# Performance work log

Measured on AMD Instinct MI355X. Metric: run time of the kernel, lower is better.

## Reference

```python
import jax, jax.numpy as jnp
import numpy as np

# Dimensions (see shape_source): B batches, W walks, L walk length, N anonymized node-id space
B, W, L, N = 256, 128, 20, 64
SIGMA = 2.0  # CooccurrenceMatrix(sigma=2.0)


def setup_inputs() -> dict:
    key = jax.random.key(0)
    k1, k2 = jax.random.split(key)
    anonymized_nodes = jax.random.randint(k1, (B, W, L), 0, N, dtype=jnp.int32)
    walk_masks = jax.random.randint(k2, (B, W, L), 0, 2).astype(bool)
    # Gaussian positional kernel buffer: kernel[i,j] = exp(-(i-j)^2 / sigma^2)
    pos = jnp.arange(L, dtype=jnp.float32)
    kernel = jnp.exp(-((pos[:, None] - pos[None, :]) ** 2) / (SIGMA ** 2))
    return {"anonymized_nodes": anonymized_nodes, "walk_masks": walk_masks, "kernel": kernel}


def reference(anonymized_nodes, walk_masks, kernel):
    # Faithful vectorized form of CooccurrenceMatrix.forward.
    # Original: per batch, group valid (walk,pos) entries by node id (sort +
    # change-points); for each group with >=2 entries, scatter-add
    # kernel[pos_i, pos_j] into cooccurrence[b, walk_i, walk_j] for all pairs
    # (i,j) in the group (including i==j). Then normalize by outer product of
    # walk lengths, clamp, tanh.
    valid = walk_masks.astype(jnp.float32)                     # [B,W,L]
    # T[b,w,l,n] = 1 if entry (w,l) is valid and holds node id n
    T = jax.nn.one_hot(anonymized_nodes, N, dtype=jnp.float32) * valid[..., None]  # [B,W,L,N]
    # Segments with < 2 occurrences contribute nothing (original skips them)
    cnt = T.sum(axis=(1, 2))                                   # [B,N]
    T = T * (cnt >= 2.0).astype(jnp.float32)[:, None, None, :]
    K = jnp.clip(kernel, -10.0, 10.0)                          # clamp as in _add_segment_deterministic
    # cooccurrence[b,w,v] = sum_n sum_{l,m} T[b,w,l,n] K[l,m] T[b,v,m,n]
    S = jnp.einsum('bwln,lm->bwmn', T, K)                      # [B,W,L,N]
    cooc = jnp.einsum('bwmn,bvmn->bwv', S, T)                  # [B,W,W]
    # Normalization by walk-length outer product
    walk_lens = valid.sum(-1)                                  # [B,W]
    norm = jnp.clip(walk_lens[:, :, None] * walk_lens[:, None, :], 1e-6, None)
    valid_pairs = (walk_lens[:, :, None] > 0) & (walk_lens[:, None, :] > 0)
    cooc = jnp.where(valid_pairs, cooc / norm, 0.0)
    return jnp.tanh(jnp.clip(cooc, -10.0, 10.0))
```

## Files before the change

kernel.cpp:

```cpp
#include <hip/hip_runtime.h>
#include <hip/hip_bf16.h>

#define BB   256
#define W    128
#define L    20
#define NN   64
#define WL   (W * L)
#define NT   1024
#define CS   129
#define NSLOT 3
#define NKEY (L * NN)
#define DLMAX 4

__global__ __launch_bounds__(NT) void cooc_kernel(
    const int* __restrict__ nodes,
    const void* __restrict__ masks,
    const float* __restrict__ kern,
    float* __restrict__ out)
{
    __shared__ __align__(16) float cooc[W * CS];
    __shared__ unsigned ent[WL];
    __shared__ unsigned hist[NKEY];
    __shared__ unsigned offs[NKEY];
    __shared__ unsigned long long maskS[40];
    __shared__ unsigned long long maskD[40];
    __shared__ int cnt[NN];
    __shared__ __align__(16) int wlen[W];
    __shared__ float diagC[W];
    __shared__ int totS;

    const int tid = threadIdx.x;
    const int b = blockIdx.x;
    const int base = b * WL;

    const unsigned mword = ((const unsigned*)masks)[tid];
    int nval[NSLOT];
    #pragma unroll
    for (int k = 0; k < NSLOT; k++) {
        int e = tid + k * NT;
        nval[k] = (e < WL) ? nodes[base + e] : 0;
    }

    hist[tid] = 0;
    if (tid + NT < NKEY) hist[tid + NT] = 0;
    {
        float4* c4 = (float4*)cooc;
        for (int i = tid; i < (W * CS) / 4; i += NT)
            c4[i] = make_float4(0.f, 0.f, 0.f, 0.f);
    }
    int flag;
    {
        unsigned v = mword;
        unsigned long long b0 = __ballot(v > 1u);
        unsigned long long b1 = __ballot(v != 0u && v != 0x3F800000u);
        unsigned long long b2 = __ballot(v != 0u && v != 0x3F80u && v != 0x3F800000u &&
                                         v != 0x3F803F80u && v != 0x3C00u &&
                                         v != 0x3C000000u && v != 0x3C003C00u);
        flag = b0 ? (b1 ? (b2 ? 1 : 3) : 2) : 0;
        flag = __builtin_amdgcn_readfirstlane(flag);
    }
    __syncthreads();

    bool vld[NSLOT];
    {
        const int e0 = tid, e1 = tid + NT, e2 = tid + 2 * NT;
        const bool g2 = (e2 < WL);
        if (flag == 0) {
            const int* m = (const int*)masks;
            vld[0] = m[base + e0] != 0;
            vld[1] = m[base + e1] != 0;
            vld[2] = g2 ? (m[base + e2] != 0) : false;
        } else if (flag == 2) {
            const float* m = (const float*)masks;
            vld[0] = m[base + e0] != 0.f;
            vld[1] = m[base + e1] != 0.f;
            vld[2] = g2 ? (m[base + e2] != 0.f) : false;
        } else if (flag == 3) {
            const unsigned short* m = (const unsigned short*)masks;
            vld[0] = m[base + e0] != 0;
            vld[1] = m[base + e1] != 0;
            vld[2] = g2 ? (m[base + e2] != 0) : false;
        } else {
            const unsigned char* m = (const unsigned char*)masks;
            vld[0] = m[base + e0] != 0;
            vld[1] = m[base + e1] != 0;
            vld[2] = g2 ? (m[base + e2] != 0) : false;
        }
    }

    unsigned eval[NSLOT];
    int      kreg[NSLOT];
    unsigned plocal[NSLOT];
    #pragma unroll
    for (int k = 0; k < NSLOT; k++) {
        int e = tid + k * NT;
        bool valid = vld[k];
        eval[k] = 0xFFFFFFFFu;
        kreg[k] = 0;
        plocal[k] = 0;
        if (valid) {
            int n = nval[k] & (NN - 1);
            int w = e / L;
            int l = e - w * L;
            eval[k] = ((unsigned)n << 12) | ((unsigned)l << 7) | (unsigned)w;
            kreg[k] = l * NN + n;
        }
        unsigned long long bal = __ballot(valid);
        int widx = k * 16 + (tid >> 6);
        if ((tid & 63) == 0 && widx < 40) maskS[widx] = bal;
        if (valid) plocal[k] = atomicAdd(&hist[kreg[k]], 1u);
    }
    __syncthreads();

    if (tid < NN) {
        int tl[L];
        int s = 0;
        #pragma unroll
        for (int l = 0; l < L; l++) { tl[l] = (int)hist[l * NN + tid]; s += tl[l]; }
        cnt[tid] = s;
        int inc = s;
        #pragma unroll
        for (int d = 1; d < NN; d <<= 1) {
            int t = __shfl_up(inc, d, 64);
            if (tid >= d) inc += t;
        }
        int run = inc - s;
        if (tid == NN - 1) totS = inc;
        #pragma unroll
        for (int l = 0; l < L; l++) {
            int idx = l * NN + tid;
            offs[idx] = (unsigned)run;
            run += tl[l];
            hist[idx] = (unsigned)run;
        }
    }
    if (tid < W) {
        int bit0 = tid * L;
        int i0 = bit0 >> 6, sh = bit0 & 63;
        unsigned long long m = maskS[i0] >> sh;
        if (sh > 64 - L) m |= maskS[i0 + 1] << (64 - sh);
        wlen[tid] = __popcll(m & 0xFFFFFu);
    }
    __syncthreads();

    #pragma unroll
    for (int k = 0; k < NSLOT; k++) {
        bool d2 = false;
        if (eval[k] != 0xFFFFFFFFu) {
            ent[offs[kreg[k]] + plocal[k]] = eval[k];
            d2 = (cnt[(int)(eval[k] >> 12)] >= 2);
        }
        unsigned long long bal = __ballot(d2);
        int widx = k * 16 + (tid >> 6);
        if ((tid & 63) == 0 && widx < 40) maskD[widx] = bal;
    }
    __syncthreads();

    if (tid < W) {
        int bit0 = tid * L;
        int i0 = bit0 >> 6, sh = bit0 & 63;
        unsigned long long m = maskD[i0] >> sh;
        if (sh > 64 - L) m |= maskD[i0 + 1] << (64 - sh);
        diagC[tid] = (float)__popcll(m & 0xFFFFFu);
    }

    const float KC = -0.360673760222f;
    const int tot = totS;
    #pragma unroll
    for (int k = 0; k < NSLOT; k++) {
        const int p = tid + k * NT;
        if (p >= tot) continue;
        const unsigned e = ent[p];
        const int n = (int)(e >> 12);
        const int l1 = (int)((e >> 7) & 31u);
        const int w1row = (int)(e & 127u) * CS;
        const int lmax = (l1 + DLMAX < L - 1) ? (l1 + DLMAX) : (L - 1);
        const int jend = (int)hist[lmax * NN + n];
        const int jm = jend - 1;
        for (int j = p + 1; j < jend; j += 4) {
            int j1 = (j + 1 < jm) ? j + 1 : jm;
            int j2 = (j + 2 < jm) ? j + 2 : jm;
            int j3 = (j + 3 < jm) ? j + 3 : jm;
            unsigned ea = ent[j];
            unsigned eb = ent[j1];
            unsigned ec = ent[j2];
            unsigned ed = ent[j3];
            int da = (int)((ea >> 7) & 31u) - l1;
            int db = (int)((eb >> 7) & 31u) - l1;
            int dc = (int)((ec >> 7) & 31u) - l1;
            int dd = (int)((ed >> 7) & 31u) - l1;
            float ka = __builtin_amdgcn_exp2f((float)(da * da) * KC);
            float kb = __builtin_amdgcn_exp2f((float)(db * db) * KC);
            float kc = __builtin_amdgcn_exp2f((float)(dc * dc) * KC);
            float kd = __builtin_amdgcn_exp2f((float)(dd * dd) * KC);
            atomicAdd(&cooc[w1row + (int)(ea & 127u)], ka);
            if (j + 1 <= jm) atomicAdd(&cooc[w1row + (int)(eb & 127u)], kb);
            if (j + 2 <= jm) atomicAdd(&cooc[w1row + (int)(ec & 127u)], kc);
            if (j + 3 <= jm) atomicAdd(&cooc[w1row + (int)(ed & 127u)], kd);
        }
    }
    __syncthreads();

    for (int s4 = 0; s4 < (W * W) / (NT * 4); s4++) {
        const int i = (tid + s4 * NT) * 4;
        const int wr = i >> 7;
        const int v = i & (W - 1);
        const float4 row = *(const float4*)&cooc[wr * CS + v];
        const int4 lv4 = *(const int4*)&wlen[v];
        const int lw = wlen[wr];
        float rr[4] = {row.x, row.y, row.z, row.w};
        float tt[4] = {cooc[(v + 0) * CS + wr], cooc[(v + 1) * CS + wr],
                       cooc[(v + 2) * CS + wr], cooc[(v + 3) * CS + wr]};
        int lv[4] = {lv4.x, lv4.y, lv4.z, lv4.w};
        float o[4];
        #pragma unroll
        for (int u = 0; u < 4; u++) {
            float s = rr[u] + tt[u];
            if (v + u == wr) s += diagC[wr];
            float nrm = (float)(lw * lv[u]);
            float x = s * __builtin_amdgcn_rcpf(fmaxf(nrm, 1e-6f));
            x = fminf(fmaxf(x, -10.f), 10.f);
            float e = __builtin_amdgcn_exp2f(x * 2.885390082f);
            float t = (e - 1.f) * __builtin_amdgcn_rcpf(e + 1.f);
            o[u] = (lw > 0 && lv[u] > 0) ? t : 0.f;
        }
        *(float4*)&out[b * W * W + i] = make_float4(o[0], o[1], o[2], o[3]);
    }
}

extern "C" void kernel_launch(void* const* d_in, const int* in_sizes, int n_in,
                              void* d_out, int out_size, void* d_ws, size_t ws_size,
                              hipStream_t stream) {
    const int*   nodes = (const int*)d_in[0];
    const void*  masks = d_in[1];
    const float* kern  = (const float*)d_in[2];
    float* out = (float*)d_out;

    cooc_kernel<<<BB, NT, 0, stream>>>(nodes, masks, kern, out);
}
```

Baseline: 75.99 us.

## Replace pairwise LDS atomics with chunked fp16 S = T·K build and gather

Rewrites the cooccurrence computation: per-walk compacted lists of repeated-node entries are built, and for each of four node chunks an fp16 LDS tensor S[l',n,w] (T convolved with the positional kernel) is accumulated. Each output pair then gathers S at the other walk's entries. This removes sorting, histogram scans and contended LDS float atomics, and uses the kernel buffer instead of a truncated exp. It adds fp16 precision loss, extra barriers per chunk and redundant full-kernel accumulation work.

```diff
diff --git a/kernel.cpp b/kernel.cpp
--- a/kernel.cpp
+++ b/kernel.cpp
@@ -1,5 +1,4 @@
 #include <hip/hip_runtime.h>
-#include <hip/hip_bf16.h>
 
 #define BB   256
 #define W    128
@@ -7,10 +6,11 @@
 #define NN   64
 #define WL   (W * L)
 #define NT   1024
-#define CS   129
 #define NSLOT 3
-#define NKEY (L * NN)
-#define DLMAX 4
+#define NC   16
+#define NCH  4
+
+typedef _Float16 h2v __attribute__((ext_vector_type(2)));
 
 __global__ __launch_bounds__(NT) void cooc_kernel(
     const int* __restrict__ nodes,
@@ -18,16 +18,14 @@
     const float* __restrict__ kern,
     float* __restrict__ out)
 {
-    __shared__ __align__(16) float cooc[W * CS];
-    __shared__ unsigned ent[WL];
-    __shared__ unsigned hist[NKEY];
-    __shared__ unsigned offs[NKEY];
+    __shared__ __align__(16) _Float16 S[L * NC * W];
+    __shared__ float Kl[L][21];
+    __shared__ unsigned short wlist[WL];
+    __shared__ unsigned char wstart[W][NCH + 1];
+    __shared__ unsigned char nodes8[WL];
     __shared__ unsigned long long maskS[40];
-    __shared__ unsigned long long maskD[40];
     __shared__ int cnt[NN];
-    __shared__ __align__(16) int wlen[W];
-    __shared__ float diagC[W];
-    __shared__ int totS;
+    __shared__ int wlen[W];
 
     const int tid = threadIdx.x;
     const int b = blockIdx.x;
@@ -40,14 +38,8 @@
         int e = tid + k * NT;
         nval[k] = (e < WL) ? nodes[base + e] : 0;
     }
-
-    hist[tid] = 0;
-    if (tid + NT < NKEY) hist[tid + NT] = 0;
-    {
-        float4* c4 = (float4*)cooc;
-        for (int i = tid; i < (W * CS) / 4; i += NT)
-            c4[i] = make_float4(0.f, 0.f, 0.f, 0.f);
-    }
+    if (tid < NN) cnt[tid] = 0;
+
     int flag;
     {
         unsigned v = mword;
@@ -64,167 +56,163 @@
     bool vld[NSLOT];
     {
         const int e0 = tid, e1 = tid + NT, e2 = tid + 2 * NT;
-        const bool g2 = (e2 < WL);
+        const bool g2v = (e2 < WL);
         if (flag == 0) {
             const int* m = (const int*)masks;
             vld[0] = m[base + e0] != 0;
             vld[1] = m[base + e1] != 0;
-            vld[2] = g2 ? (m[base + e2] != 0) : false;
+            vld[2] = g2v ? (m[base + e2] != 0) : false;
         } else if (flag == 2) {
             const float* m = (const float*)masks;
             vld[0] = m[base + e0] != 0.f;
             vld[1] = m[base + e1] != 0.f;
-            vld[2] = g2 ? (m[base + e2] != 0.f) : false;
+            vld[2] = g2v ? (m[base + e2] != 0.f) : false;
         } else if (flag == 3) {
             const unsigned short* m = (const unsigned short*)masks;
             vld[0] = m[base + e0] != 0;
             vld[1] = m[base + e1] != 0;
-            vld[2] = g2 ? (m[base + e2] != 0) : false;
+            vld[2] = g2v ? (m[base + e2] != 0) : false;
         } else {
             const unsigned char* m = (const unsigned char*)masks;
             vld[0] = m[base + e0] != 0;
             vld[1] = m[base + e1] != 0;
-            vld[2] = g2 ? (m[base + e2] != 0) : false;
-        }
-    }
-
-    unsigned eval[NSLOT];
-    int      kreg[NSLOT];
-    unsigned plocal[NSLOT];
+            vld[2] = g2v ? (m[base + e2] != 0) : false;
+        }
+    }
+
     #pragma unroll
     for (int k = 0; k < NSLOT; k++) {
         int e = tid + k * NT;
         bool valid = vld[k];
-        eval[k] = 0xFFFFFFFFu;
-        kreg[k] = 0;
-        plocal[k] = 0;
-        if (valid) {
-            int n = nval[k] & (NN - 1);
-            int w = e / L;
-            int l = e - w * L;
-            eval[k] = ((unsigned)n << 12) | ((unsigned)l << 7) | (unsigned)w;
-            kreg[k] = l * NN + n;
-        }
+        int n = nval[k] & (NN - 1);
+        if (e < WL) nodes8[e] = (unsigned char)n;
         unsigned long long bal = __ballot(valid);
         int widx = k * 16 + (tid >> 6);
         if ((tid & 63) == 0 && widx < 40) maskS[widx] = bal;
-        if (valid) plocal[k] = atomicAdd(&hist[kreg[k]], 1u);
+        if (valid) atomicAdd(&cnt[n], 1);
     }
     __syncthreads();
 
-    if (tid < NN) {
-        int tl[L];
-        int s = 0;
+    if (tid < W) {
+        const int w = tid;
+        int bit0 = w * L;
+        int i0 = bit0 >> 6, sh = bit0 & 63;
+        unsigned long long mm = maskS[i0] >> sh;
+        if (sh > 64 - L) mm |= maskS[i0 + 1] << (64 - sh);
+        unsigned v20 = (unsigned)(mm & 0xFFFFFu);
+        wlen[w] = __popc(v20);
+        unsigned long long c4 = 0;
+        unsigned t = v20;
+        while (t) {
+            int l = __ffs(t) - 1; t &= t - 1;
+            int n = nodes8[w * L + l];
+            if (cnt[n] >= 2) c4 += 1ull << (16 * (n >> 4));
+        }
+        unsigned o1 = (unsigned)(c4 & 0xFFFFu);
+        unsigned o2 = o1 + (unsigned)((c4 >> 16) & 0xFFFFu);
+        unsigned o3 = o2 + (unsigned)((c4 >> 32) & 0xFFFFu);
+        unsigned o4 = o3 + (unsigned)((c4 >> 48) & 0xFFFFu);
+        wstart[w][0] = 0;
+        wstart[w][1] = (unsigned char)o1;
+        wstart[w][2] = (unsigned char)o2;
+        wstart[w][3] = (unsigned char)o3;
+        wstart[w][4] = (unsigned char)o4;
+        unsigned long long cur = ((unsigned long long)o1 << 16) |
+                                 ((unsigned long long)o2 << 32) |
+                                 ((unsigned long long)o3 << 48);
+        t = v20;
+        while (t) {
+            int l = __ffs(t) - 1; t &= t - 1;
+            int n = nodes8[w * L + l];
+            if (cnt[n] >= 2) {
+                int c = n >> 4;
+                unsigned off = (unsigned)((cur >> (16 * c)) & 0xFFFFu);
+                wlist[w * L + off] = (unsigned short)((l << 4) | (n & 15));
+                cur += 1ull << (16 * c);
+            }
+        }
+    } else {
+        int idx = tid - W;
+        if (idx < L * 21) {
+            int r = idx / 21, cc = idx - r * 21;
+            float kv = (cc < L) ? kern[r * L + cc] : 0.f;
+            Kl[r][cc] = fminf(fmaxf(kv, -10.f), 10.f);
+        }
+        float4 z4 = make_float4(0.f, 0.f, 0.f, 0.f);
+        float4* s4 = (float4*)S;
+        for (int i = tid - W; i < 5120; i += NT - W) s4[i] = z4;
+    }
+    __syncthreads();
+
+    const int gw = tid >> 7;
+    const int wb = tid & (W - 1);
+    const int lpLo = (5 * gw) >> 1;
+    const int lpHi = (5 * (gw + 1)) >> 1;
+    const int w1p = tid & 63;
+    const int g2 = tid >> 6;
+
+    float accx[8], accy[8];
+    #pragma unroll
+    for (int i = 0; i < 8; i++) { accx[i] = 0.f; accy[i] = 0.f; }
+
+    for (int c = 0; c < NCH; c++) {
+        {
+            const int jb = wb * L + wstart[wb][c];
+            const int je = wb * L + wstart[wb][c + 1];
+            for (int j = jb; j < je; j++) {
+                const unsigned val = wlist[j];
+                const int le = (int)(val >> 4);
+                const int nl = (int)(val & 15u);
+                for (int lp = lpLo; lp < lpHi; lp++) {
+                    const float kv = Kl[le][lp];
+                    const int idx = ((lp << 4) | nl) * W + wb;
+                    S[idx] = (_Float16)((float)S[idx] + kv);
+                }
+            }
+        }
+        __syncthreads();
         #pragma unroll
-        for (int l = 0; l < L; l++) { tl[l] = (int)hist[l * NN + tid]; s += tl[l]; }
-        cnt[tid] = s;
-        int inc = s;
-        #pragma unroll
-        for (int d = 1; d < NN; d <<= 1) {
-            int t = __shfl_up(inc, d, 64);
-            if (tid >= d) inc += t;
-        }
-        int run = inc - s;
-        if (tid == NN - 1) totS = inc;
-        #pragma unroll
-        for (int l = 0; l < L; l++) {
-            int idx = l * NN + tid;
-            offs[idx] = (unsigned)run;
-            run += tl[l];
-            hist[idx] = (unsigned)run;
-        }
-    }
-    if (tid < W) {
-        int bit0 = tid * L;
-        int i0 = bit0 >> 6, sh = bit0 & 63;
-        unsigned long long m = maskS[i0] >> sh;
-        if (sh > 64 - L) m |= maskS[i0 + 1] << (64 - sh);
-        wlen[tid] = __popcll(m & 0xFFFFFu);
-    }
-    __syncthreads();
-
-    #pragma unroll
-    for (int k = 0; k < NSLOT; k++) {
-        bool d2 = false;
-        if (eval[k] != 0xFFFFFFFFu) {
-            ent[offs[kreg[k]] + plocal[k]] = eval[k];
-            d2 = (cnt[(int)(eval[k] >> 12)] >= 2);
-        }
-        unsigned long long bal = __ballot(d2);
-        int widx = k * 16 + (tid >> 6);
-        if ((tid & 63) == 0 && widx < 40) maskD[widx] = bal;
-    }
-    __syncthreads();
-
-    if (tid < W) {
-        int bit0 = tid * L;
-        int i0 = bit0 >> 6, sh = bit0 & 63;
-        unsigned long long m = maskD[i0] >> sh;
-        if (sh > 64 - L) m |= maskD[i0 + 1] << (64 - sh);
-        diagC[tid] = (float)__popcll(m & 0xFFFFFu);
-    }
-
-    const float KC = -0.360673760222f;
-    const int tot = totS;
-    #pragma unroll
-    for (int k = 0; k < NSLOT; k++) {
-        const int p = tid + k * NT;
-        if (p >= tot) continue;
-        const unsigned e = ent[p];
-        const int n = (int)(e >> 12);
-        const int l1 = (int)((e >> 7) & 31u);
-        const int w1row = (int)(e & 127u) * CS;
-        const int lmax = (l1 + DLMAX < L - 1) ? (l1 + DLMAX) : (L - 1);
-        const int jend = (int)hist[lmax * NN + n];
-        const int jm = jend - 1;
-        for (int j = p + 1; j < jend; j += 4) {
-            int j1 = (j + 1 < jm) ? j + 1 : jm;
-            int j2 = (j + 2 < jm) ? j + 2 : jm;
-            int j3 = (j + 3 < jm) ? j + 3 : jm;
-            unsigned ea = ent[j];
-            unsigned eb = ent[j1];
-            unsigned ec = ent[j2];
-            unsigned ed = ent[j3];
-            int da = (int)((ea >> 7) & 31u) - l1;
-            int db = (int)((eb >> 7) & 31u) - l1;
-            int dc = (int)((ec >> 7) & 31u) - l1;
-            int dd = (int)((ed >> 7) & 31u) - l1;
-            float ka = __builtin_amdgcn_exp2f((float)(da * da) * KC);
-            float kb = __builtin_amdgcn_exp2f((float)(db * db) * KC);
-            float kc = __builtin_amdgcn_exp2f((float)(dc * dc) * KC);
-            float kd = __builtin_amdgcn_exp2f((float)(dd * dd) * KC);
-            atomicAdd(&cooc[w1row + (int)(ea & 127u)], ka);
-            if (j + 1 <= jm) atomicAdd(&cooc[w1row + (int)(eb & 127u)], kb);
-            if (j + 2 <= jm) atomicAdd(&cooc[w1row + (int)(ec & 127u)], kc);
-            if (j + 3 <= jm) atomicAdd(&cooc[w1row + (int)(ed & 127u)], kd);
-        }
-    }
-    __syncthreads();
-
-    for (int s4 = 0; s4 < (W * W) / (NT * 4); s4++) {
-        const int i = (tid + s4 * NT) * 4;
-        const int wr = i >> 7;
-        const int v = i & (W - 1);
-        const float4 row = *(const float4*)&cooc[wr * CS + v];
-        const int4 lv4 = *(const int4*)&wlen[v];
-        const int lw = wlen[wr];
-        float rr[4] = {row.x, row.y, row.z, row.w};
-        float tt[4] = {cooc[(v + 0) * CS + wr], cooc[(v + 1) * CS + wr],
-                       cooc[(v + 2) * CS + wr], cooc[(v + 3) * CS + wr]};
-        int lv[4] = {lv4.x, lv4.y, lv4.z, lv4.w};
-        float o[4];
-        #pragma unroll
-        for (int u = 0; u < 4; u++) {
-            float s = rr[u] + tt[u];
-            if (v + u == wr) s += diagC[wr];
-            float nrm = (float)(lw * lv[u]);
-            float x = s * __builtin_amdgcn_rcpf(fmaxf(nrm, 1e-6f));
-            x = fminf(fmaxf(x, -10.f), 10.f);
-            float e = __builtin_amdgcn_exp2f(x * 2.885390082f);
-            float t = (e - 1.f) * __builtin_amdgcn_rcpf(e + 1.f);
-            o[u] = (lw > 0 && lv[u] > 0) ? t : 0.f;
-        }
-        *(float4*)&out[b * W * W + i] = make_float4(o[0], o[1], o[2], o[3]);
+        for (int i = 0; i < 8; i++) {
+            const int w2 = g2 * 8 + i;
+            const int jb = w2 * L + wstart[w2][c];
+            const int je = w2 * L + wstart[w2][c + 1];
+            for (int j = jb; j < je; j++) {
+                const unsigned val = wlist[j];
+                const h2v hv = *(const h2v*)&S[(int)val * W + 2 * w1p];
+                accx[i] += (float)hv[0];
+                accy[i] += (float)hv[1];
+            }
+        }
+        __syncthreads();
+        if (c < NCH - 1) {
+            float4 z4 = make_float4(0.f, 0.f, 0.f, 0.f);
+            float4* s4 = (float4*)S;
+            #pragma unroll
+            for (int i = 0; i < 5; i++) s4[tid + i * NT] = z4;
+            __syncthreads();
+        }
+    }
+
+    const int lwa = wlen[2 * w1p];
+    const int lwb = wlen[2 * w1p + 1];
+    const float fa = (float)lwa, fb = (float)lwb;
+    float* po = out + b * W * W;
+    #pragma unroll
+    for (int i = 0; i < 8; i++) {
+        const int w2 = g2 * 8 + i;
+        const int lv = wlen[w2];
+        const float fv = (float)lv;
+        float xa = accx[i] * __builtin_amdgcn_rcpf(fmaxf(fv * fa, 1e-6f));
+        float xb = accy[i] * __builtin_amdgcn_rcpf(fmaxf(fv * fb, 1e-6f));
+        xa = fminf(fmaxf(xa, -10.f), 10.f);
+        xb = fminf(fmaxf(xb, -10.f), 10.f);
+        const float ea = __builtin_amdgcn_exp2f(xa * 2.885390082f);
+        const float eb = __builtin_amdgcn_exp2f(xb * 2.885390082f);
+        float oa = (ea - 1.f) * __builtin_amdgcn_rcpf(ea + 1.f);
+        float ob = (eb - 1.f) * __builtin_amdgcn_rcpf(eb + 1.f);
+        oa = (lv > 0 && lwa > 0) ? oa : 0.f;
+        ob = (lv > 0 && lwb > 0) ? ob : 0.f;
+        *(float2*)&po[w2 * W + 2 * w1p] = make_float2(oa, ob);
     }
 }
 
```

Measured after the change: 92.76 us. 22.1% more time.
